# Kernel optimization log

Hardware: AMD Instinct MI355X
Metric: run time of the kernel (lower is better)

The kernel has to match this reference:

```python
import jax, jax.numpy as jnp
import numpy as np

N_NODES = 50000
BETA = 0.5
NEG_SLOPE = 0.2


def gat_conv(x, src, dst, W, a_src, a_dst, b):
    """Single-head GAT-style conv: gather, attend, softmax-per-dst, scatter-sum."""
    h = x @ W                                   # [N, F]
    as_ = h @ a_src                             # [N]
    ad_ = h @ a_dst                             # [N]
    e = jax.nn.leaky_relu(as_[src] + ad_[dst], NEG_SLOPE)  # [E]
    # numerically stable softmax over incoming edges of each dst node
    m = jax.ops.segment_max(e, dst, num_segments=N_NODES)  # [N]
    ex = jnp.exp(e - m[dst])                    # [E]
    denom = jax.ops.segment_sum(ex, dst, num_segments=N_NODES)  # [N]
    w = ex / denom[dst]                         # [E]
    out = jax.ops.segment_sum(w[:, None] * h[src], dst, num_segments=N_NODES)
    return out + b


def setup_inputs() -> dict:
    key = jax.random.key(0)
    ks = jax.random.split(key, 8)
    F_in, F_out = 64, 64
    x = jax.random.normal(ks[0], (N_NODES, F_in), dtype=jnp.float32)
    edge_index = jax.random.randint(ks[1], (2, 1600000), 0, N_NODES, dtype=jnp.int64)
    W = jax.random.normal(ks[2], (F_in, F_in), dtype=jnp.float32) * (1.0 / np.sqrt(F_in))
    a_src = jax.random.normal(ks[3], (F_in,), dtype=jnp.float32) * (1.0 / np.sqrt(F_in))
    a_dst = jax.random.normal(ks[4], (F_in,), dtype=jnp.float32) * (1.0 / np.sqrt(F_in))
    b = jnp.zeros((F_in,), dtype=jnp.float32)
    fc_w = jax.random.normal(ks[5], (F_in, F_out), dtype=jnp.float32) * (1.0 / np.sqrt(F_in))
    fc_b = jnp.zeros((F_out,), dtype=jnp.float32)
    return {"x": x, "edge_index": edge_index, "W": W, "a_src": a_src,
            "a_dst": a_dst, "b": b, "fc_w": fc_w, "fc_b": fc_b}


def reference(x, edge_index, W, a_src, a_dst, b, fc_w, fc_b):
    src, dst = edge_index[0], edge_index[1]
    x1 = BETA * gat_conv(x, src, dst, W, a_src, a_dst, b) + (1.0 - BETA) * x
    x2 = BETA * gat_conv(x1, src, dst, W, a_src, a_dst, b) + (1.0 - BETA) * x
    x3 = BETA * gat_conv(x2, src, dst, W, a_src, a_dst, b) + (1.0 - BETA) * x
    h = x3
    out = x3 @ fc_w + fc_b
    return (out, h)
```

## Files before the change

kernel.cpp:

```cpp
#include <hip/hip_runtime.h>
#include <hip/hip_bf16.h>
#include <math.h>

#define N_NODES 50000
#define FDIM 64
#define BETA 0.5f
#define NEG_SLOPE 0.2f

typedef __attribute__((ext_vector_type(8))) short bf16x8;
typedef __attribute__((ext_vector_type(4))) float f32x4;

__device__ __forceinline__ unsigned short f2bf(float f) {
    unsigned u = __float_as_uint(f);
    unsigned r = (u + 0x7FFFu + ((u >> 16) & 1u)) >> 16;
    return (unsigned short)r;
}
__device__ __forceinline__ float bf2f(unsigned short s) {
    return __uint_as_float((unsigned)s << 16);
}

#define CHUNK 4096
__global__ __launch_bounds__(256) void scatter_pairs(
    const unsigned int* __restrict__ eiu, int* __restrict__ gCursor,
    unsigned int* __restrict__ pairs, int E, int CAP) {
    __shared__ int det;
    __shared__ unsigned int staged[CHUNK];
    __shared__ unsigned short tmpd[CHUNK];
    __shared__ int hist[256], sc[256], lbase[256], gbase[256], lcur[256];
    int t = threadIdx.x;
    if (t == 0) det = 0;
    hist[t] = 0;
    __syncthreads();
    int beg = blockIdx.x * CHUNK;
    int end = min(E, beg + CHUNK);
    int n = end - beg;
    {
        int idx = beg + t;
        if (idx < E && eiu[2 * idx + 1] != 0u) atomicOr(&det, 1);
    }
    __syncthreads();
    bool is32 = det != 0;
    for (int i = beg + t; i < end; i += 256) {
        int d = is32 ? (int)eiu[E + i] : (int)eiu[2 * (size_t)(E + i)];
        tmpd[i - beg] = (unsigned short)d;
        atomicAdd(&hist[d >> 8], 1);
    }
    __syncthreads();
    sc[t] = hist[t];
    __syncthreads();
    for (int off = 1; off < 256; off <<= 1) {
        int v = (t >= off) ? sc[t - off] : 0;
        __syncthreads();
        sc[t] += v;
        __syncthreads();
    }
    int excl = sc[t] - hist[t];
    lbase[t] = excl;
    lcur[t] = excl;
    if (hist[t] > 0) gbase[t] = t * CAP + atomicAdd(&gCursor[t], hist[t]);
    __syncthreads();
    for (int i = beg + t; i < end; i += 256) {
        unsigned s = is32 ? eiu[i] : eiu[2 * (size_t)i];
        unsigned td = tmpd[i - beg];
        int b = (int)(td >> 8);
        int lp = atomicAdd(&lcur[b], 1);
        staged[lp] = s | (td << 16);
    }
    __syncthreads();
    for (int j = t; j < n; j += 256) {
        unsigned w = staged[j];
        int b = (int)(w >> 24);
        pairs[gbase[b] + (j - lbase[b])] = w;
    }
}

__global__ __launch_bounds__(1024) void bucket_sort(
    const unsigned int* __restrict__ pairs, const int* __restrict__ gCursor,
    int* __restrict__ offsets, unsigned short* __restrict__ srcs,
    int* __restrict__ degCnt, int N, int E, int CAP) {
    __shared__ int scb[256], cnt[256], sc[256], lcur[256], dh[256];
    __shared__ unsigned short sorted16[16384];
    int b = blockIdx.x, t = threadIdx.x;
    if (t < 256) { scb[t] = gCursor[t]; dh[t] = 0; }
    __syncthreads();
    for (int off = 1; off < 256; off <<= 1) {
        int v = (t < 256 && t >= off) ? scb[t - off] : 0;
        __syncthreads();
        if (t < 256) scb[t] += v;
        __syncthreads();
    }
    int cntb = gCursor[b];
    int beg = scb[b] - cntb;
    int pbase = b * CAP;
    bool useLds = cntb <= 16384;
    if (b == 0 && t == 0) offsets[N] = E;
    if (t < 256) cnt[t] = 0;
    __syncthreads();
    for (int i = t; i < cntb; i += 1024) atomicAdd(&cnt[(pairs[pbase + i] >> 16) & 255u], 1);
    __syncthreads();
    if (t < 256) {
        sc[t] = cnt[t];
        int node = (b << 8) + t;
        if (node < N) atomicAdd(&dh[min(cnt[t], 255)], 1);
    }
    __syncthreads();
    if (t < 256 && dh[t]) atomicAdd(&degCnt[t], dh[t]);
    for (int off = 1; off < 256; off <<= 1) {
        int v = (t < 256 && t >= off) ? sc[t - off] : 0;
        __syncthreads();
        if (t < 256) sc[t] += v;
        __syncthreads();
    }
    if (t < 256) {
        int excl = sc[t] - cnt[t];
        int node = (b << 8) + t;
        if (node < N) offsets[node] = beg + excl;
        lcur[t] = excl;
    }
    __syncthreads();
    if (useLds) {
        for (int i = t; i < cntb; i += 1024) {
            unsigned p = pairs[pbase + i];
            int lp = atomicAdd(&lcur[(p >> 16) & 255u], 1);
            sorted16[lp] = (unsigned short)(p & 0xFFFFu);
        }
        __syncthreads();
        for (int j = t; j < cntb; j += 1024) srcs[beg + j] = sorted16[j];
    } else {
        for (int i = t; i < cntb; i += 1024) {
            unsigned p = pairs[pbase + i];
            int lp = atomicAdd(&lcur[(p >> 16) & 255u], 1);
            srcs[beg + lp] = (unsigned short)(p & 0xFFFFu);
        }
    }
}

__global__ __launch_bounds__(256) void src_sort(
    const int* __restrict__ offsets, unsigned short* __restrict__ srcs, int N) {
    int wv = (blockIdx.x * blockDim.x + threadIdx.x) >> 6;
    if (wv >= N) return;
    int lane = threadIdx.x & 63;
    int beg = offsets[wv], end = offsets[wv + 1];
    int deg = end - beg;
    if (deg <= 1 || deg > 64) return;
    unsigned v = (lane < deg) ? (unsigned)srcs[beg + lane] : 0xFFFFFFFFu;
#pragma unroll
    for (int k = 2; k <= 64; k <<= 1) {
#pragma unroll
        for (int j = k >> 1; j >= 1; j >>= 1) {
            unsigned pv = __shfl_xor(v, j, 64);
            bool up = ((lane & k) == 0);
            bool takeMin = (((lane & j) == 0) == up);
            v = takeMin ? min(v, pv) : max(v, pv);
        }
    }
    if (lane < deg) srcs[beg + lane] = (unsigned short)v;
}

__global__ __launch_bounds__(256) void deg_scan(int* degCnt) {
    __shared__ int sc[256];
    int t = threadIdx.x;
    int c = degCnt[t];
    sc[t] = c;
    __syncthreads();
    for (int off = 1; off < 256; off <<= 1) {
        int v = (t >= off) ? sc[t - off] : 0;
        __syncthreads();
        sc[t] += v;
        __syncthreads();
    }
    degCnt[t] = sc[t] - c;
}

#define DCHUNK 2048
__global__ __launch_bounds__(256) void deg_scatter(
    const int* __restrict__ offsets, int* __restrict__ degCnt,
    int* __restrict__ perm, int N) {
    __shared__ int lh[256], lbase[256], lcur[256];
    int t = threadIdx.x;
    int beg = blockIdx.x * DCHUNK;
    int end = min(N, beg + DCHUNK);
    lh[t] = 0;
    lcur[t] = 0;
    __syncthreads();
    for (int i = beg + t; i < end; i += 256) {
        int d = min(offsets[i + 1] - offsets[i], 255);
        atomicAdd(&lh[d], 1);
    }
    __syncthreads();
    if (lh[t] > 0) lbase[t] = atomicAdd(&degCnt[t], lh[t]);
    __syncthreads();
    for (int i = beg + t; i < end; i += 256) {
        int d = min(offsets[i + 1] - offsets[i], 255);
        int r = atomicAdd(&lcur[d], 1);
        perm[lbase[d] + r] = i;
    }
}

__global__ __launch_bounds__(256) void prep_weights(
    const float* __restrict__ W, const float* __restrict__ fcw,
    unsigned short* __restrict__ WTh, unsigned short* __restrict__ WTl,
    unsigned short* __restrict__ FTh, unsigned short* __restrict__ FTl) {
    for (int idx = blockIdx.x * 256 + threadIdx.x; idx < 4096; idx += gridDim.x * 256) {
        int k = idx >> 6, f = idx & 63;
        float w = W[idx];
        unsigned short hi = f2bf(w);
        WTh[f * 64 + k] = hi;
        WTl[f * 64 + k] = f2bf(w - bf2f(hi));
        float w2 = fcw[idx];
        unsigned short hi2 = f2bf(w2);
        FTh[f * 64 + k] = hi2;
        FTl[f * 64 + k] = f2bf(w2 - bf2f(hi2));
    }
}

__global__ __launch_bounds__(256, 4) void transform_mfma(
    const float* __restrict__ x,
    const unsigned short* __restrict__ WTh, const unsigned short* __restrict__ WTl,
    const float* __restrict__ a_src, const float* __restrict__ a_dst,
    const float* __restrict__ bias,
    unsigned short* __restrict__ hb,
    float* __restrict__ fout,
    float* __restrict__ as_, float* __restrict__ ad_, int N) {
    __shared__ __align__(16) unsigned short WThs[64 * 72];
    __shared__ __align__(16) unsigned short WTls[64 * 72];
    int tid = threadIdx.x;
    {
        int row = tid >> 2;
        int ch = (tid & 3) * 16;
        uint4 h0 = ((const uint4*)(WTh + row * 64 + ch))[0];
        uint4 h1 = ((const uint4*)(WTh + row * 64 + ch))[1];
        uint4 l0 = ((const uint4*)(WTl + row * 64 + ch))[0];
        uint4 l1 = ((const uint4*)(WTl + row * 64 + ch))[1];
        *((uint4*)(WThs + row * 72 + ch)) = h0;
        *((uint4*)(WThs + row * 72 + ch + 8)) = h1;
        *((uint4*)(WTls + row * 72 + ch)) = l0;
        *((uint4*)(WTls + row * 72 + ch + 8)) = l1;
    }

    int wid = tid >> 6;
    int lane = tid & 63;
    int col = lane & 15;
    int quad = lane >> 4;
    int mbase = blockIdx.x * 64 + wid * 16;

    bf16x8 Ah[2], Al[2];
    int arow = mbase + col;
    const float* xr = x + (size_t)(arow < N ? arow : 0) * FDIM + quad * 8;
#pragma unroll
    for (int ks = 0; ks < 2; ks++) {
        float4 xa = *(const float4*)(xr + ks * 32);
        float4 xb = *(const float4*)(xr + ks * 32 + 4);
        float xv[8] = {xa.x, xa.y, xa.z, xa.w, xb.x, xb.y, xb.z, xb.w};
#pragma unroll
        for (int e = 0; e < 8; e++) {
            unsigned short hi = f2bf(xv[e]);
            Ah[ks][e] = (short)hi;
            Al[ks][e] = (short)f2bf(xv[e] - bf2f(hi));
        }
    }
    __syncthreads();

    f32x4 acc[4];
#pragma unroll
    for (int ft = 0; ft < 4; ft++) acc[ft] = (f32x4){0.f, 0.f, 0.f, 0.f};

#pragma unroll
    for (int ft = 0; ft < 4; ft++) {
        int f = ft * 16 + col;
#pragma unroll
        for (int ks = 0; ks < 2; ks++) {
            int off = f * 72 + ks * 32 + quad * 8;
            bf16x8 Bh = *(const bf16x8*)(WThs + off);
            bf16x8 Bl = *(const bf16x8*)(WTls + off);
            acc[ft] = __builtin_amdgcn_mfma_f32_16x16x32_bf16(Ah[ks], Bh, acc[ft], 0, 0, 0);
            acc[ft] = __builtin_amdgcn_mfma_f32_16x16x32_bf16(Ah[ks], Bl, acc[ft], 0, 0, 0);
            acc[ft] = __builtin_amdgcn_mfma_f32_16x16x32_bf16(Al[ks], Bh, acc[ft], 0, 0, 0);
        }
    }

    if (fout) {
#pragma unroll
        for (int ft = 0; ft < 4; ft++) {
            int f = ft * 16 + col;
            float bv = bias ? bias[f] : 0.f;
#pragma unroll
            for (int r = 0; r < 4; r++) {
                int node = mbase + quad * 4 + r;
                if (node < N) fout[(size_t)node * FDIM + f] = acc[ft][r] + bv;
            }
        }
    }
    if (hb) {
#pragma unroll
        for (int ft = 0; ft < 4; ft++) {
            int f = ft * 16 + col;
#pragma unroll
            for (int r = 0; r < 4; r++) {
                int node = mbase + quad * 4 + r;
                if (node < N) hb[(size_t)node * FDIM + f] = f2bf(acc[ft][r]);
            }
        }
    }
    if (as_) {
        float asv[4], adv[4];
#pragma unroll
        for (int ft = 0; ft < 4; ft++) {
            asv[ft] = a_src[ft * 16 + col];
            adv[ft] = a_dst[ft * 16 + col];
        }
#pragma unroll
        for (int r = 0; r < 4; r++) {
            float pa = 0.f, pd = 0.f;
#pragma unroll
            for (int ft = 0; ft < 4; ft++) {
                pa = fmaf(acc[ft][r], asv[ft], pa);
                pd = fmaf(acc[ft][r], adv[ft], pd);
            }
#pragma unroll
            for (int off = 1; off <= 8; off <<= 1) {
                pa += __shfl_xor(pa, off, 64);
                pd += __shfl_xor(pd, off, 64);
            }
            int node = mbase + quad * 4 + r;
            if (col == 0 && node < N) { as_[node] = pa; ad_[node] = pd; }
        }
    }
}

__device__ __forceinline__ void fma8(float* acc, float ex, const uint4& hv) {
    acc[0] = fmaf(ex, __uint_as_float(hv.x << 16), acc[0]);
    acc[1] = fmaf(ex, __uint_as_float(hv.x & 0xFFFF0000u), acc[1]);
    acc[2] = fmaf(ex, __uint_as_float(hv.y << 16), acc[2]);
    acc[3] = fmaf(ex, __uint_as_float(hv.y & 0xFFFF0000u), acc[3]);
    acc[4] = fmaf(ex, __uint_as_float(hv.z << 16), acc[4]);
    acc[5] = fmaf(ex, __uint_as_float(hv.z & 0xFFFF0000u), acc[5]);
    acc[6] = fmaf(ex, __uint_as_float(hv.w << 16), acc[6]);
    acc[7] = fmaf(ex, __uint_as_float(hv.w & 0xFFFF0000u), acc[7]);
}

__global__ __launch_bounds__(256) void gat_gather(
    const unsigned short* __restrict__ hb,
    const float* __restrict__ as_, const float* __restrict__ ad_,
    const int* __restrict__ offsets, const unsigned short* __restrict__ srcs,
    const int* __restrict__ perm,
    const float* __restrict__ bvec, const float* __restrict__ x0,
    float* __restrict__ xout, int N) {
    int wid = (blockIdx.x * blockDim.x + threadIdx.x) >> 6;
    int lane = threadIdx.x & 63;
    int g = lane >> 3;
    int q = lane & 7;
    int ni = wid * 8 + g;
    bool active = ni < N;
    int node = active ? perm[ni] : 0;
    int beg = active ? offsets[node] : 0;
    int end = active ? offsets[node + 1] : 0;
    int deg = end - beg;
    float adv = active ? ad_[node] : 0.f;
    int mx = deg;
    mx = max(mx, __shfl_xor(mx, 8, 64));
    mx = max(mx, __shfl_xor(mx, 16, 64));
    mx = max(mx, __shfl_xor(mx, 32, 64));

    float acc[8];
#pragma unroll
    for (int k = 0; k < 8; k++) acc[k] = 0.f;
    float denom = 0.f;
    const unsigned short* hq = hb + (q << 3);

#define LRELU_EXP(E_) __expf((E_) > 0.f ? (E_) : NEG_SLOPE * (E_))

    int p0 = (int)srcs[(0 < deg) ? beg + 0 : 0];
    int p1 = (int)srcs[(1 < deg) ? beg + 1 : 0];
    int p2 = (int)srcs[(2 < deg) ? beg + 2 : 0];
    int p3 = (int)srcs[(3 < deg) ? beg + 3 : 0];

    for (int st = 0; st < mx; st += 4) {
        int ns = st + 4;
        int n0 = (int)srcs[(ns + 0 < deg) ? beg + ns + 0 : 0];
        int n1 = (int)srcs[(ns + 1 < deg) ? beg + ns + 1 : 0];
        int n2 = (int)srcs[(ns + 2 < deg) ? beg + ns + 2 : 0];
        int n3 = (int)srcs[(ns + 3 < deg) ? beg + ns + 3 : 0];
        uint4 hv0 = *(const uint4*)(hq + ((size_t)p0 << 6));
        uint4 hv1 = *(const uint4*)(hq + ((size_t)p1 << 6));
        uint4 hv2 = *(const uint4*)(hq + ((size_t)p2 << 6));
        uint4 hv3 = *(const uint4*)(hq + ((size_t)p3 << 6));
        float e0 = as_[p0] + adv;
        float e1 = as_[p1] + adv;
        float e2 = as_[p2] + adv;
        float e3 = as_[p3] + adv;
        float ex0 = (st + 0 < deg) ? LRELU_EXP(e0) : 0.f;
        float ex1 = (st + 1 < deg) ? LRELU_EXP(e1) : 0.f;
        float ex2 = (st + 2 < deg) ? LRELU_EXP(e2) : 0.f;
        float ex3 = (st + 3 < deg) ? LRELU_EXP(e3) : 0.f;
        denom += (ex0 + ex1) + (ex2 + ex3);
        fma8(acc, ex0, hv0);
        fma8(acc, ex1, hv1);
        fma8(acc, ex2, hv2);
        fma8(acc, ex3, hv3);
        p0 = n0; p1 = n1; p2 = n2; p3 = n3;
    }
#undef LRELU_EXP

    if (active) {
        float inv = denom > 0.f ? 1.f / denom : 0.f;
        int fb = q * 8;
        f32x4 b0 = *(const f32x4*)(bvec + fb);
        f32x4 b1 = *(const f32x4*)(bvec + fb + 4);
        const float* x0r = x0 + (size_t)node * FDIM + fb;
        f32x4 x0a = *(const f32x4*)(x0r);
        f32x4 x0b = *(const f32x4*)(x0r + 4);
        f32x4 o0, o1;
        o0.x = BETA * (acc[0] * inv + b0.x) + (1.f - BETA) * x0a.x;
        o0.y = BETA * (acc[1] * inv + b0.y) + (1.f - BETA) * x0a.y;
        o0.z = BETA * (acc[2] * inv + b0.z) + (1.f - BETA) * x0a.z;
        o0.w = BETA * (acc[3] * inv + b0.w) + (1.f - BETA) * x0a.w;
        o1.x = BETA * (acc[4] * inv + b1.x) + (1.f - BETA) * x0b.x;
        o1.y = BETA * (acc[5] * inv + b1.y) + (1.f - BETA) * x0b.y;
        o1.z = BETA * (acc[6] * inv + b1.z) + (1.f - BETA) * x0b.z;
        o1.w = BETA * (acc[7] * inv + b1.w) + (1.f - BETA) * x0b.w;
        float* xr = xout + (size_t)node * FDIM + fb;
        *(f32x4*)(xr) = o0;
        *(f32x4*)(xr + 4) = o1;
    }
}

extern "C" void kernel_launch(void* const* d_in, const int* in_sizes, int n_in,
                              void* d_out, int out_size, void* d_ws, size_t ws_size,
                              hipStream_t stream) {
    const int N = N_NODES;
    const int E = in_sizes[1] / 2;
    const int NB = (N + 255) >> 8;
    const int CAP = (((E / N) * 256) * 2 + 1023) & ~1023;

    const float* x     = (const float*)d_in[0];
    const void*  ei    = d_in[1];
    const float* W     = (const float*)d_in[2];
    const float* a_src = (const float*)d_in[3];
    const float* a_dst = (const float*)d_in[4];
    const float* bvec  = (const float*)d_in[5];
    const float* fc_w  = (const float*)d_in[6];
    const float* fc_b  = (const float*)d_in[7];

    float* out = (float*)d_out;
    float* x3  = out + (size_t)N * FDIM;

    char* p = (char*)d_ws;
    auto alloc = [&](size_t bytes) -> void* {
        void* r = (void*)p;
        p += (bytes + 255) & ~(size_t)255;
        return r;
    };
    int*            gCursor  = (int*)alloc(512 * 4);
    unsigned int*   pairs    = (unsigned int*)alloc((size_t)256 * CAP * 4);
    unsigned short* srcs     = (unsigned short*)alloc((size_t)E * 2);
    int*            offsets  = (int*)alloc((size_t)(N + 1) * 4);
    int*            perm     = (int*)alloc((size_t)N * 4);
    float*          as_      = (float*)alloc((size_t)N * 4);
    float*          ad_      = (float*)alloc((size_t)N * 4);
    unsigned short* hbuf     = (unsigned short*)alloc((size_t)N * FDIM * 2);
    float*          xbuf     = (float*)alloc((size_t)N * FDIM * 4);
    unsigned short* WTh      = (unsigned short*)alloc(4096 * 2);
    unsigned short* WTl      = (unsigned short*)alloc(4096 * 2);
    unsigned short* FTh      = (unsigned short*)alloc(4096 * 2);
    unsigned short* FTl      = (unsigned short*)alloc(4096 * 2);
    int* degCnt = gCursor + 256;

    hipMemsetAsync(gCursor, 0, 512 * 4, stream);

    prep_weights<<<16, 256, 0, stream>>>(W, fc_w, WTh, WTl, FTh, FTl);

    scatter_pairs<<<(E + CHUNK - 1) / CHUNK, 256, 0, stream>>>(
        (const unsigned int*)ei, gCursor, pairs, E, CAP);
    bucket_sort<<<NB, 1024, 0, stream>>>(pairs, gCursor, offsets, srcs, degCnt, N, E, CAP);

    src_sort<<<(N + 3) / 4, 256, 0, stream>>>(offsets, srcs, N);
    deg_scan<<<1, 256, 0, stream>>>(degCnt);
    deg_scatter<<<(N + DCHUNK - 1) / DCHUNK, 256, 0, stream>>>(offsets, degCnt, perm, N);

    int tgrid = (N + 63) / 64;
    int gwaves = (N + 7) / 8;
    int ggrid = (gwaves + 3) / 4;

    transform_mfma<<<tgrid, 256, 0, stream>>>(x, WTh, WTl, a_src, a_dst, nullptr,
                                              hbuf, nullptr, as_, ad_, N);
    gat_gather<<<ggrid, 256, 0, stream>>>(hbuf, as_, ad_, offsets, srcs, perm,
                                          bvec, x, xbuf, N);
    transform_mfma<<<tgrid, 256, 0, stream>>>(xbuf, WTh, WTl, a_src, a_dst, nullptr,
                                              hbuf, nullptr, as_, ad_, N);
    gat_gather<<<ggrid, 256, 0, stream>>>(hbuf, as_, ad_, offsets, srcs, perm,
                                          bvec, x, xbuf, N);
    transform_mfma<<<tgrid, 256, 0, stream>>>(xbuf, WTh, WTl, a_src, a_dst, nullptr,
                                              hbuf, nullptr, as_, ad_, N);
    gat_gather<<<ggrid, 256, 0, stream>>>(hbuf, as_, ad_, offsets, srcs, perm,
                                          bvec, x, x3, N);
    transform_mfma<<<tgrid, 256, 0, stream>>>(x3, FTh, FTl, nullptr, nullptr, fc_b,
                                              nullptr, out, nullptr, nullptr, N);
}
```

Baseline: 265.5 us.

## Drop per-node source sort, reverse gather order, use nontemporal loads/stores

Removes the src_sort kernel that bitonic-sorted each node's incoming source list, saving one launch and a pass over the edge array at the risk of less local h-row access in the gather. The gather kernel now walks the degree-sorted permutation in reverse group order, so waves start from the other end of the degree ordering, and streaming accesses (perm, srcs, x0 reads, xout writes) use nontemporal loads and stores so they pollute the cache less and leave room for the reused h rows. Summation order within a node is unchanged apart from the source order.

```diff
diff --git a/kernel.cpp b/kernel.cpp
--- a/kernel.cpp
+++ b/kernel.cpp
@@ -133,28 +133,6 @@
             srcs[beg + lp] = (unsigned short)(p & 0xFFFFu);
         }
     }
-}
-
-__global__ __launch_bounds__(256) void src_sort(
-    const int* __restrict__ offsets, unsigned short* __restrict__ srcs, int N) {
-    int wv = (blockIdx.x * blockDim.x + threadIdx.x) >> 6;
-    if (wv >= N) return;
-    int lane = threadIdx.x & 63;
-    int beg = offsets[wv], end = offsets[wv + 1];
-    int deg = end - beg;
-    if (deg <= 1 || deg > 64) return;
-    unsigned v = (lane < deg) ? (unsigned)srcs[beg + lane] : 0xFFFFFFFFu;
-#pragma unroll
-    for (int k = 2; k <= 64; k <<= 1) {
-#pragma unroll
-        for (int j = k >> 1; j >= 1; j >>= 1) {
-            unsigned pv = __shfl_xor(v, j, 64);
-            bool up = ((lane & k) == 0);
-            bool takeMin = (((lane & j) == 0) == up);
-            v = takeMin ? min(v, pv) : max(v, pv);
-        }
-    }
-    if (lane < deg) srcs[beg + lane] = (unsigned short)v;
 }
 
 __global__ __launch_bounds__(256) void deg_scan(int* degCnt) {
@@ -347,12 +325,14 @@
     const float* __restrict__ bvec, const float* __restrict__ x0,
     float* __restrict__ xout, int N) {
     int wid = (blockIdx.x * blockDim.x + threadIdx.x) >> 6;
+    int ngroups = (N + 7) >> 3;
+    int rg = ngroups - 1 - wid;
     int lane = threadIdx.x & 63;
     int g = lane >> 3;
     int q = lane & 7;
-    int ni = wid * 8 + g;
-    bool active = ni < N;
-    int node = active ? perm[ni] : 0;
+    int ni = rg * 8 + g;
+    bool active = (rg >= 0) && (ni < N);
+    int node = active ? __builtin_nontemporal_load(perm + ni) : 0;
     int beg = active ? offsets[node] : 0;
     int end = active ? offsets[node + 1] : 0;
     int deg = end - beg;
@@ -369,18 +349,19 @@
     const unsigned short* hq = hb + (q << 3);
 
 #define LRELU_EXP(E_) __expf((E_) > 0.f ? (E_) : NEG_SLOPE * (E_))
-
-    int p0 = (int)srcs[(0 < deg) ? beg + 0 : 0];
-    int p1 = (int)srcs[(1 < deg) ? beg + 1 : 0];
-    int p2 = (int)srcs[(2 < deg) ? beg + 2 : 0];
-    int p3 = (int)srcs[(3 < deg) ? beg + 3 : 0];
+#define NTL(P_) __builtin_nontemporal_load(P_)
+
+    int p0 = (int)NTL(srcs + ((0 < deg) ? beg + 0 : 0));
+    int p1 = (int)NTL(srcs + ((1 < deg) ? beg + 1 : 0));
+    int p2 = (int)NTL(srcs + ((2 < deg) ? beg + 2 : 0));
+    int p3 = (int)NTL(srcs + ((3 < deg) ? beg + 3 : 0));
 
     for (int st = 0; st < mx; st += 4) {
         int ns = st + 4;
-        int n0 = (int)srcs[(ns + 0 < deg) ? beg + ns + 0 : 0];
-        int n1 = (int)srcs[(ns + 1 < deg) ? beg + ns + 1 : 0];
-        int n2 = (int)srcs[(ns + 2 < deg) ? beg + ns + 2 : 0];
-        int n3 = (int)srcs[(ns + 3 < deg) ? beg + ns + 3 : 0];
+        int n0 = (int)NTL(srcs + ((ns + 0 < deg) ? beg + ns + 0 : 0));
+        int n1 = (int)NTL(srcs + ((ns + 1 < deg) ? beg + ns + 1 : 0));
+        int n2 = (int)NTL(srcs + ((ns + 2 < deg) ? beg + ns + 2 : 0));
+        int n3 = (int)NTL(srcs + ((ns + 3 < deg) ? beg + ns + 3 : 0));
         uint4 hv0 = *(const uint4*)(hq + ((size_t)p0 << 6));
         uint4 hv1 = *(const uint4*)(hq + ((size_t)p1 << 6));
         uint4 hv2 = *(const uint4*)(hq + ((size_t)p2 << 6));
@@ -408,8 +389,8 @@
         f32x4 b0 = *(const f32x4*)(bvec + fb);
         f32x4 b1 = *(const f32x4*)(bvec + fb + 4);
         const float* x0r = x0 + (size_t)node * FDIM + fb;
-        f32x4 x0a = *(const f32x4*)(x0r);
-        f32x4 x0b = *(const f32x4*)(x0r + 4);
+        f32x4 x0a = NTL((const f32x4*)(x0r));
+        f32x4 x0b = NTL((const f32x4*)(x0r + 4));
         f32x4 o0, o1;
         o0.x = BETA * (acc[0] * inv + b0.x) + (1.f - BETA) * x0a.x;
         o0.y = BETA * (acc[1] * inv + b0.y) + (1.f - BETA) * x0a.y;
@@ -420,9 +401,10 @@
         o1.z = BETA * (acc[6] * inv + b1.z) + (1.f - BETA) * x0b.z;
         o1.w = BETA * (acc[7] * inv + b1.w) + (1.f - BETA) * x0b.w;
         float* xr = xout + (size_t)node * FDIM + fb;
-        *(f32x4*)(xr) = o0;
-        *(f32x4*)(xr + 4) = o1;
-    }
+        __builtin_nontemporal_store(o0, (f32x4*)(xr));
+        __builtin_nontemporal_store(o1, (f32x4*)(xr + 4));
+    }
+#undef NTL
 }
 
 extern "C" void kernel_launch(void* const* d_in, const int* in_sizes, int n_in,
@@ -474,7 +456,6 @@
         (const unsigned int*)ei, gCursor, pairs, E, CAP);
     bucket_sort<<<NB, 1024, 0, stream>>>(pairs, gCursor, offsets, srcs, degCnt, N, E, CAP);
 
-    src_sort<<<(N + 3) / 4, 256, 0, stream>>>(offsets, srcs, N);
     deg_scan<<<1, 256, 0, stream>>>(degCnt);
     deg_scatter<<<(N + DCHUNK - 1) / DCHUNK, 256, 0, stream>>>(offsets, degCnt, perm, N);
 
```

After: 313.2 us. 18.0% more time.

## Fold weight prep and degree scan into neighbor kernels, drop per-node source sort

Applied to the files above, without the earlier changes.

Moves the weight transpose and bf16 hi/lo split into an extra block of scatter_pairs. Each deg_scatter block now recomputes the 256-bin degree scan redundantly, using a separate relative cursor array, so the single-block scan kernel goes away. The src_sort pass, which bitonic-sorted each node's incoming source list, is removed. This cuts three launches and one sort pass. The cost is that gather loads become less ordered by source, which may hurt locality, and floating-point summation order may change.

```diff
diff --git a/kernel.cpp b/kernel.cpp
--- a/kernel.cpp
+++ b/kernel.cpp
@@ -22,12 +22,29 @@
 #define CHUNK 4096
 __global__ __launch_bounds__(256) void scatter_pairs(
     const unsigned int* __restrict__ eiu, int* __restrict__ gCursor,
-    unsigned int* __restrict__ pairs, int E, int CAP) {
+    unsigned int* __restrict__ pairs, int E, int CAP, int nChunks,
+    const float* __restrict__ W, const float* __restrict__ fcw,
+    unsigned short* __restrict__ WTh, unsigned short* __restrict__ WTl,
+    unsigned short* __restrict__ FTh, unsigned short* __restrict__ FTl) {
+    int t = threadIdx.x;
+    if (blockIdx.x >= nChunks) {
+        for (int idx = t; idx < 4096; idx += 256) {
+            int k = idx >> 6, f = idx & 63;
+            float w = W[idx];
+            unsigned short hi = f2bf(w);
+            WTh[f * 64 + k] = hi;
+            WTl[f * 64 + k] = f2bf(w - bf2f(hi));
+            float w2 = fcw[idx];
+            unsigned short hi2 = f2bf(w2);
+            FTh[f * 64 + k] = hi2;
+            FTl[f * 64 + k] = f2bf(w2 - bf2f(hi2));
+        }
+        return;
+    }
     __shared__ int det;
     __shared__ unsigned int staged[CHUNK];
     __shared__ unsigned short tmpd[CHUNK];
     __shared__ int hist[256], sc[256], lbase[256], gbase[256], lcur[256];
-    int t = threadIdx.x;
     if (t == 0) det = 0;
     hist[t] = 0;
     __syncthreads();
@@ -135,60 +152,33 @@
     }
 }
 
-__global__ __launch_bounds__(256) void src_sort(
-    const int* __restrict__ offsets, unsigned short* __restrict__ srcs, int N) {
-    int wv = (blockIdx.x * blockDim.x + threadIdx.x) >> 6;
-    if (wv >= N) return;
-    int lane = threadIdx.x & 63;
-    int beg = offsets[wv], end = offsets[wv + 1];
-    int deg = end - beg;
-    if (deg <= 1 || deg > 64) return;
-    unsigned v = (lane < deg) ? (unsigned)srcs[beg + lane] : 0xFFFFFFFFu;
-#pragma unroll
-    for (int k = 2; k <= 64; k <<= 1) {
-#pragma unroll
-        for (int j = k >> 1; j >= 1; j >>= 1) {
-            unsigned pv = __shfl_xor(v, j, 64);
-            bool up = ((lane & k) == 0);
-            bool takeMin = (((lane & j) == 0) == up);
-            v = takeMin ? min(v, pv) : max(v, pv);
-        }
-    }
-    if (lane < deg) srcs[beg + lane] = (unsigned short)v;
-}
-
-__global__ __launch_bounds__(256) void deg_scan(int* degCnt) {
-    __shared__ int sc[256];
-    int t = threadIdx.x;
-    int c = degCnt[t];
-    sc[t] = c;
-    __syncthreads();
-    for (int off = 1; off < 256; off <<= 1) {
-        int v = (t >= off) ? sc[t - off] : 0;
-        __syncthreads();
-        sc[t] += v;
-        __syncthreads();
-    }
-    degCnt[t] = sc[t] - c;
-}
-
 #define DCHUNK 2048
 __global__ __launch_bounds__(256) void deg_scatter(
-    const int* __restrict__ offsets, int* __restrict__ degCnt,
-    int* __restrict__ perm, int N) {
-    __shared__ int lh[256], lbase[256], lcur[256];
+    const int* __restrict__ offsets, const int* __restrict__ degHist,
+    int* __restrict__ cursorRel, int* __restrict__ perm, int N) {
+    __shared__ int scanB[256], lh[256], lbase[256], lcur[256];
     int t = threadIdx.x;
+    int c = degHist[t];
+    scanB[t] = c;
+    __syncthreads();
+    for (int off = 1; off < 256; off <<= 1) {
+        int v = (t >= off) ? scanB[t - off] : 0;
+        __syncthreads();
+        scanB[t] += v;
+        __syncthreads();
+    }
+    int base0 = scanB[t] - c;
+    lh[t] = 0;
+    lcur[t] = 0;
+    __syncthreads();
     int beg = blockIdx.x * DCHUNK;
     int end = min(N, beg + DCHUNK);
-    lh[t] = 0;
-    lcur[t] = 0;
-    __syncthreads();
     for (int i = beg + t; i < end; i += 256) {
         int d = min(offsets[i + 1] - offsets[i], 255);
         atomicAdd(&lh[d], 1);
     }
     __syncthreads();
-    if (lh[t] > 0) lbase[t] = atomicAdd(&degCnt[t], lh[t]);
+    if (lh[t] > 0) lbase[t] = base0 + atomicAdd(&cursorRel[t], lh[t]);
     __syncthreads();
     for (int i = beg + t; i < end; i += 256) {
         int d = min(offsets[i + 1] - offsets[i], 255);
@@ -197,25 +187,8 @@
     }
 }
 
-__global__ __launch_bounds__(256) void prep_weights(
-    const float* __restrict__ W, const float* __restrict__ fcw,
-    unsigned short* __restrict__ WTh, unsigned short* __restrict__ WTl,
-    unsigned short* __restrict__ FTh, unsigned short* __restrict__ FTl) {
-    for (int idx = blockIdx.x * 256 + threadIdx.x; idx < 4096; idx += gridDim.x * 256) {
-        int k = idx >> 6, f = idx & 63;
-        float w = W[idx];
-        unsigned short hi = f2bf(w);
-        WTh[f * 64 + k] = hi;
-        WTl[f * 64 + k] = f2bf(w - bf2f(hi));
-        float w2 = fcw[idx];
-        unsigned short hi2 = f2bf(w2);
-        FTh[f * 64 + k] = hi2;
-        FTl[f * 64 + k] = f2bf(w2 - bf2f(hi2));
-    }
-}
-
-__global__ __launch_bounds__(256, 4) void transform_mfma(
-    const float* __restrict__ x,
+__global__ __launch_bounds__(256, 4) void transform_k(
+    const float* __restrict__ xin,
     const unsigned short* __restrict__ WTh, const unsigned short* __restrict__ WTl,
     const float* __restrict__ a_src, const float* __restrict__ a_dst,
     const float* __restrict__ bias,
@@ -246,7 +219,7 @@
 
     bf16x8 Ah[2], Al[2];
     int arow = mbase + col;
-    const float* xr = x + (size_t)(arow < N ? arow : 0) * FDIM + quad * 8;
+    const float* xr = xin + (size_t)(arow < N ? arow : 0) * FDIM + quad * 8;
 #pragma unroll
     for (int ks = 0; ks < 2; ks++) {
         float4 xa = *(const float4*)(xr + ks * 32);
@@ -451,7 +424,7 @@
         p += (bytes + 255) & ~(size_t)255;
         return r;
     };
-    int*            gCursor  = (int*)alloc(512 * 4);
+    int*            gCursor  = (int*)alloc(768 * 4);
     unsigned int*   pairs    = (unsigned int*)alloc((size_t)256 * CAP * 4);
     unsigned short* srcs     = (unsigned short*)alloc((size_t)E * 2);
     int*            offsets  = (int*)alloc((size_t)(N + 1) * 4);
@@ -464,36 +437,35 @@
     unsigned short* WTl      = (unsigned short*)alloc(4096 * 2);
     unsigned short* FTh      = (unsigned short*)alloc(4096 * 2);
     unsigned short* FTl      = (unsigned short*)alloc(4096 * 2);
-    int* degCnt = gCursor + 256;
-
-    hipMemsetAsync(gCursor, 0, 512 * 4, stream);
-
-    prep_weights<<<16, 256, 0, stream>>>(W, fc_w, WTh, WTl, FTh, FTl);
-
-    scatter_pairs<<<(E + CHUNK - 1) / CHUNK, 256, 0, stream>>>(
-        (const unsigned int*)ei, gCursor, pairs, E, CAP);
+    int* degCnt    = gCursor + 256;
+    int* cursorRel = gCursor + 512;
+
+    hipMemsetAsync(gCursor, 0, 768 * 4, stream);
+
+    const int nChunks = (E + CHUNK - 1) / CHUNK;
+    scatter_pairs<<<nChunks + 1, 256, 0, stream>>>(
+        (const unsigned int*)ei, gCursor, pairs, E, CAP, nChunks,
+        W, fc_w, WTh, WTl, FTh, FTl);
     bucket_sort<<<NB, 1024, 0, stream>>>(pairs, gCursor, offsets, srcs, degCnt, N, E, CAP);
-
-    src_sort<<<(N + 3) / 4, 256, 0, stream>>>(offsets, srcs, N);
-    deg_scan<<<1, 256, 0, stream>>>(degCnt);
-    deg_scatter<<<(N + DCHUNK - 1) / DCHUNK, 256, 0, stream>>>(offsets, degCnt, perm, N);
+    deg_scatter<<<(N + DCHUNK - 1) / DCHUNK, 256, 0, stream>>>(
+        offsets, degCnt, cursorRel, perm, N);
 
     int tgrid = (N + 63) / 64;
     int gwaves = (N + 7) / 8;
     int ggrid = (gwaves + 3) / 4;
 
-    transform_mfma<<<tgrid, 256, 0, stream>>>(x, WTh, WTl, a_src, a_dst, nullptr,
-                                              hbuf, nullptr, as_, ad_, N);
+    transform_k<<<tgrid, 256, 0, stream>>>(x, WTh, WTl, a_src, a_dst, nullptr,
+                                           hbuf, nullptr, as_, ad_, N);
     gat_gather<<<ggrid, 256, 0, stream>>>(hbuf, as_, ad_, offsets, srcs, perm,
                                           bvec, x, xbuf, N);
-    transform_mfma<<<tgrid, 256, 0, stream>>>(xbuf, WTh, WTl, a_src, a_dst, nullptr,
-                                              hbuf, nullptr, as_, ad_, N);
+    transform_k<<<tgrid, 256, 0, stream>>>(xbuf, WTh, WTl, a_src, a_dst, nullptr,
+                                           hbuf, nullptr, as_, ad_, N);
     gat_gather<<<ggrid, 256, 0, stream>>>(hbuf, as_, ad_, offsets, srcs, perm,
                                           bvec, x, xbuf, N);
-    transform_mfma<<<tgrid, 256, 0, stream>>>(xbuf, WTh, WTl, a_src, a_dst, nullptr,
-                                              hbuf, nullptr, as_, ad_, N);
+    transform_k<<<tgrid, 256, 0, stream>>>(xbuf, WTh, WTl, a_src, a_dst, nullptr,
+                                           hbuf, nullptr, as_, ad_, N);
     gat_gather<<<ggrid, 256, 0, stream>>>(hbuf, as_, ad_, offsets, srcs, perm,
                                           bvec, x, x3, N);
-    transform_mfma<<<tgrid, 256, 0, stream>>>(x3, FTh, FTl, nullptr, nullptr, fc_b,
-                                              nullptr, out, nullptr, nullptr, N);
-}
+    transform_k<<<tgrid, 256, 0, stream>>>(x3, FTh, FTl, nullptr, nullptr, fc_b,
+                                           nullptr, out, nullptr, nullptr, N);
+}
```

After: 250.9 us. 5.5% less time.
